# Performance work log

Hardware: AMD Instinct MI355X
Metric: run time of the kernel (lower is better)

The kernel has to match this reference:

```python
import jax, jax.numpy as jnp
import numpy as np
from jax import lax

H = 256  # hidden_size


def _conv1d(x, w, b):
    # x: (N, Cin, L), w: (Cout, Cin, K) -> (N, Cout, L-K+1), VALID, stride 1
    y = lax.conv_general_dilated(x, w, window_strides=(1,), padding='VALID',
                                 dimension_numbers=('NCH', 'OIH', 'NCH'))
    return y + b[None, :, None]


def _gru_dir(x, Wih, Whh, bih, bhh):
    # x: (L, N, H). Torch GRU cell equations.
    L, N, _ = x.shape
    gi = jnp.einsum('lnh,gh->lng', x, Wih) + bih  # (L, N, 3H) precomputed input gates
    h0 = jnp.zeros((N, H), x.dtype)

    def step(h, gi_t):
        gh = h @ Whh.T + bhh                       # (N, 3H)
        ir, iz, inn = jnp.split(gi_t, 3, axis=-1)
        hr, hz, hn = jnp.split(gh, 3, axis=-1)
        r = jax.nn.sigmoid(ir + hr)
        z = jax.nn.sigmoid(iz + hz)
        n = jnp.tanh(inn + r * hn)
        h_new = (1.0 - z) * n + z * h
        return h_new, h_new

    hT, ys = lax.scan(step, h0, gi)
    return ys, hT  # (L, N, H), (N, H)


def setup_inputs() -> dict:
    key = jax.random.key(0)
    ks = jax.random.split(key, 14)
    N, C, L = 32, 13, 4096
    s = 0.1
    inp = {
        'X': jax.random.normal(ks[0], (N, C, L), jnp.float32),
        'W1': jax.random.normal(ks[1], (H // 2, C, 3), jnp.float32) * s,
        'b1': jax.random.normal(ks[2], (H // 2,), jnp.float32) * s,
        'W2': jax.random.normal(ks[3], (H, H // 2, 3), jnp.float32) * s,
        'b2': jax.random.normal(ks[4], (H,), jnp.float32) * s,
        'Wih_f': jax.random.normal(ks[5], (3 * H, H), jnp.float32) * s,
        'Whh_f': jax.random.normal(ks[6], (3 * H, H), jnp.float32) * s,
        'bih_f': jax.random.normal(ks[7], (3 * H,), jnp.float32) * s,
        'bhh_f': jax.random.normal(ks[8], (3 * H,), jnp.float32) * s,
        'Wih_b': jax.random.normal(ks[9], (3 * H, H), jnp.float32) * s,
        'Whh_b': jax.random.normal(ks[10], (3 * H, H), jnp.float32) * s,
        'bih_b': jax.random.normal(ks[11], (3 * H,), jnp.float32) * s,
        'bhh_b': jax.random.normal(ks[12], (3 * H,), jnp.float32) * s,
    }
    return inp


def reference(X, W1, b1, W2, b2, Wih_f, Whh_f, bih_f, bhh_f,
              Wih_b, Whh_b, bih_b, bhh_b):
    # dropouts are identity in eval mode; N>1 so squeeze() is a no-op
    x = _conv1d(X, W1, b1)           # (N, H/2, L-2)
    x = _conv1d(x, W2, b2)           # (N, H,   L-4)
    x = x[:, :, ::2]                 # MaxPool1d(kernel=1, stride=2) == stride-2 subsample
    x = jnp.transpose(x, (2, 0, 1))  # (L', N, H)

    out_f, hT_f = _gru_dir(x, Wih_f, Whh_f, bih_f, bhh_f)
    # backward direction: reverse time, scan, reverse outputs
    out_b_rev, hT_b = _gru_dir(x[::-1], Wih_b, Whh_b, bih_b, bhh_b)
    out_b = out_b_rev[::-1]

    # original: fwd + flip(bwd along FEATURE axis), averaged, ReLU (faithful to np.flip(axis=-1))
    comb = jax.nn.relu((out_f + out_b[:, :, ::-1]) * 0.5)  # (L', N, H)
    hidden_last = hT_b[None]                                # hidden[-1].unsqueeze(0): (1, N, H)
    return comb, hidden_last
```

## Files before the change

kernel.cpp:

```cpp
#include <hip/hip_runtime.h>
#include <hip/hip_fp16.h>
#include <cstdint>
#include <cstddef>

#define L_SEQ 2046
#define NBATCH 32
#define HID 256
#define M_PAD 65536

typedef _Float16 h2vec  __attribute__((ext_vector_type(2)));
typedef _Float16 half8v __attribute__((ext_vector_type(8)));
typedef float    f32x4  __attribute__((ext_vector_type(4)));

static __device__ __forceinline__ uint32_t pack2(float a, float b) {
  __half2 h = __floats2half2_rn(a, b);
  return __builtin_bit_cast(uint32_t, h);
}

static __device__ __forceinline__ float fdot2u(uint32_t w, uint32_t h, float c) {
#if __has_builtin(__builtin_amdgcn_fdot2)
  return __builtin_amdgcn_fdot2(__builtin_bit_cast(h2vec, w),
                                __builtin_bit_cast(h2vec, h), c, false);
#else
  __half2 a = __builtin_bit_cast(__half2, w);
  __half2 b = __builtin_bit_cast(__half2, h);
  float2 fa = __half22float2(a), fb = __half22float2(b);
  return c + fa.x * fb.x + fa.y * fb.y;
#endif
}

static __device__ __forceinline__ void gload_lds16(const void* g, void* l) {
  __builtin_amdgcn_global_load_lds(
      (const __attribute__((address_space(1))) void*)g,
      (__attribute__((address_space(3))) void*)l, 16, 0, 0);
}

__global__ void k_conv_im2col(const float* __restrict__ X,
                              const float* __restrict__ W1,
                              const float* __restrict__ b1,
                              __half* __restrict__ A1h) {
  int j   = threadIdx.x;
  int row = blockIdx.x;
  int l2 = row >> 5, n = row & 31;
  float v = 0.f;
  if (l2 < L_SEQ) {
    int ci = j / 3;
    int k  = j - 3 * ci;
    int p  = 2 * l2 + k;
    const float* xb = X + (size_t)n * 13 * 4096 + p;
    const float* w  = W1 + ci * 39;
    float acc = b1[ci];
#pragma unroll
    for (int c = 0; c < 13; c++) {
      const float* xp = xb + (size_t)c * 4096;
      acc += xp[0] * w[3*c+0] + xp[1] * w[3*c+1] + xp[2] * w[3*c+2];
    }
    v = acc;
  }
  A1h[(size_t)row * 384 + j] = __float2half(v);
}

__global__ void k_cvt_h(const float* __restrict__ src, __half* __restrict__ dst,
                        int nelem) {
  int i = blockIdx.x * 256 + threadIdx.x;
  if (i < nelem) dst[i] = __float2half(src[i]);
}

__global__ __launch_bounds__(256, 3) void k_gemm_mfma(
    const __half* __restrict__ A, const __half* __restrict__ Bh,
    const float* __restrict__ bias, __half* __restrict__ C,
    int K, int ldC, int col_off) {
  __shared__ __half Asl[128 * 64];
  __shared__ __half Bsl[128 * 64];
  const int tid  = threadIdx.x;
  const int wave = tid >> 6, lane = tid & 63;
  const int m_blk = blockIdx.x * 128;
  const int n_blk = blockIdx.y * 128;
  const int wm = wave >> 1, wn = wave & 1;

  f32x4 acc[4][4];
#pragma unroll
  for (int i = 0; i < 4; i++)
#pragma unroll
    for (int j = 0; j < 4; j++) acc[i][j] = (f32x4)0.f;

  int srow[4], sko[4];
#pragma unroll
  for (int i = 0; i < 4; i++) {
    int s = (i * 4 + wave) * 64 + lane;
    srow[i] = s >> 3;
    sko[i]  = (s & 7) ^ ((s >> 3) & 7);
  }

  for (int kc = 0; kc < K; kc += 64) {
#pragma unroll
    for (int i = 0; i < 4; i++) {
      int s = (i * 4 + wave) * 64 + lane;
      gload_lds16(A + (size_t)(m_blk + srow[i]) * K + kc + sko[i] * 8,
                  &Asl[s * 8]);
    }
#pragma unroll
    for (int i = 0; i < 4; i++) {
      int s = (i * 4 + wave) * 64 + lane;
      gload_lds16(Bh + (size_t)(n_blk + srow[i]) * K + kc + sko[i] * 8,
                  &Bsl[s * 8]);
    }
    __syncthreads();
#pragma unroll
    for (int kb = 0; kb < 2; kb++) {
      half8v af[4], bf[4];
#pragma unroll
      for (int mi = 0; mi < 4; mi++) {
        int row = wm * 64 + mi * 16 + (lane & 15);
        int c   = (kb * 4 + (lane >> 4)) ^ (row & 7);
        af[mi] = *(const half8v*)&Asl[row * 64 + c * 8];
      }
#pragma unroll
      for (int ni = 0; ni < 4; ni++) {
        int row = wn * 64 + ni * 16 + (lane & 15);
        int c   = (kb * 4 + (lane >> 4)) ^ (row & 7);
        bf[ni] = *(const half8v*)&Bsl[row * 64 + c * 8];
      }
#pragma unroll
      for (int mi = 0; mi < 4; mi++)
#pragma unroll
        for (int ni = 0; ni < 4; ni++)
          acc[mi][ni] = __builtin_amdgcn_mfma_f32_16x16x32_f16(
              af[mi], bf[ni], acc[mi][ni], 0, 0, 0);
    }
    __syncthreads();
  }
#pragma unroll
  for (int ni = 0; ni < 4; ni++) {
    int col = wn * 64 + ni * 16 + (lane & 15);
    float bj = bias[n_blk + col];
#pragma unroll
    for (int mi = 0; mi < 4; mi++) {
      int row0 = m_blk + wm * 64 + mi * 16 + (lane >> 4) * 4;
#pragma unroll
      for (int r = 0; r < 4; r++) {
        C[(size_t)(row0 + r) * ldC + col_off + n_blk + col] =
            __float2half(acc[mi][ni][r] + bj);
      }
    }
  }
}

__global__ void k_packw2(const float* __restrict__ Whh_f,
                         const float* __restrict__ Whh_b,
                         uint4* __restrict__ Wpk) {
  int idx = blockIdx.x * 256 + threadIdx.x;
  int d   = idx / 24576;
  int r   = idx - d * 24576;
  int w   = r / 768;
  int j   = r - w * 768;
  const float* W = d ? Whh_b : Whh_f;
  const float* src = W + (size_t)j * 256 + w * 8;
  uint4 o;
  o.x = pack2(src[0], src[1]);
  o.y = pack2(src[2], src[3]);
  o.z = pack2(src[4], src[5]);
  o.w = pack2(src[6], src[7]);
  Wpk[(size_t)idx] = o;
}

__global__ __attribute__((amdgpu_flat_work_group_size(768, 768),
                          amdgpu_waves_per_eu(3, 3)))
void k_gru(
    const __half* __restrict__ gih, const uint4* __restrict__ Wpk,
    const float* __restrict__ bhh_f, const float* __restrict__ bhh_b,
    float* __restrict__ outF, __half* __restrict__ outBh,
    float* __restrict__ hT) {
  const int blk = blockIdx.x;
  const int dir = blk >> 5;
  const int n   = blk & 31;
  const int tid = threadIdx.x;
  const int wv_ = tid >> 6;
  const int lane = tid & 63;
  const bool is_act = (wv_ % 3) == 0;
  const int g = (wv_ / 3) * 64 + lane;

  const float* bhh = dir ? bhh_b : bhh_f;

  uint4 wv[32];
  {
    const uint4* wp = Wpk + (size_t)dir * 24576 + tid;
#pragma unroll
    for (int w = 0; w < 32; w++) wv[w] = wp[w * 768];
#pragma unroll
    for (int w = 0; w < 32; w++) {
      asm volatile("" : "+v"(wv[w].x), "+v"(wv[w].y), "+v"(wv[w].z), "+v"(wv[w].w));
    }
  }
  const float bh0 = bhh[g];
  const float bh1 = bhh[256 + g];
  const float bh2 = bhh[512 + g];

  __shared__ __align__(16) __half hs[2][256];
  __shared__ float a_lds[768];
  if (tid < 128) ((uint32_t*)hs)[tid] = 0u;
  float hp = 0.f;

  const __half* gr = gih + ((size_t)(dir ? (size_t)(L_SEQ - 1) * NBATCH : 0) + n) * 1536
                         + dir * 768 + g;
  const ptrdiff_t gstep = dir ? -(ptrdiff_t)(NBATCH * 1536) : (ptrdiff_t)(NBATCH * 1536);
  __half pi0 = __float2half(0.f), pi1 = pi0, pi2 = pi0;
  if (is_act) { pi0 = gr[0]; pi1 = gr[256]; pi2 = gr[512]; }
  __syncthreads();

  for (int t = 0; t < L_SEQ; t++) {
    const uint4* hb = (const uint4*)hs[t & 1];
    float a = 0.f;
#pragma unroll
    for (int w = 0; w < 32; w++) {
      uint4 hq = hb[w];
      uint4 u  = wv[w];
      a = fdot2u(u.x, hq.x, a);
      a = fdot2u(u.y, hq.y, a);
      a = fdot2u(u.z, hq.z, a);
      a = fdot2u(u.w, hq.w, a);
    }
    a_lds[tid] = a;
    __syncthreads();

    if (is_act) {
      float hr = a_lds[g]       + bh0;
      float hz = a_lds[256 + g] + bh1;
      float hn = a_lds[512 + g] + bh2;
      float ir  = __half2float(pi0);
      float iz  = __half2float(pi1);
      float inn = __half2float(pi2);
      float rr = 1.f / (1.f + __expf(-(ir + hr)));
      float zz = 1.f / (1.f + __expf(-(iz + hz)));
      float e  = __expf(2.f * (inn + rr * hn));
      float nn = 1.f - 2.f / (e + 1.f);
      float hnew = (1.f - zz) * nn + zz * hp;
      hp = hnew;
      __half hh = __float2half(hnew);
      hs[(t + 1) & 1][g] = hh;
      const int l = dir ? (L_SEQ - 1 - t) : t;
      uint32_t oi = ((uint32_t)l * NBATCH + n) * HID + g;
      if (dir == 0) outF[oi] = hnew;
      else          outBh[oi] = hh;
      gr += gstep;
      if (t + 1 < L_SEQ) { pi0 = gr[0]; pi1 = gr[256]; pi2 = gr[512]; }
    }
    __syncthreads();
  }
  if (dir == 1 && is_act) hT[n * HID + g] = hp;
}

__global__ void k_combine(float* __restrict__ outF,
                          const __half* __restrict__ outBh) {
  int idx = blockIdx.x * 256 + threadIdx.x;
  int c = idx & 255;
  float v = 0.5f * (outF[idx] + __half2float(outBh[idx + 255 - 2 * c]));
  outF[idx] = v > 0.f ? v : 0.f;
}

extern "C" void kernel_launch(void* const* d_in, const int* in_sizes, int n_in,
                              void* d_out, int out_size, void* d_ws, size_t ws_size,
                              hipStream_t stream) {
  const float* X     = (const float*)d_in[0];
  const float* W1    = (const float*)d_in[1];
  const float* b1    = (const float*)d_in[2];
  const float* W2    = (const float*)d_in[3];
  const float* b2    = (const float*)d_in[4];
  const float* Wih_f = (const float*)d_in[5];
  const float* Whh_f = (const float*)d_in[6];
  const float* bih_f = (const float*)d_in[7];
  const float* bhh_f = (const float*)d_in[8];
  const float* Wih_b = (const float*)d_in[9];
  const float* Whh_b = (const float*)d_in[10];
  const float* bih_b = (const float*)d_in[11];
  const float* bhh_b = (const float*)d_in[12];

  char* wsb = (char*)d_ws;
  __half* gih   = (__half*)(wsb);
  __half* W2h   = (__half*)(wsb);
  __half* A1h   = (__half*)(wsb + 201326592);
  __half* outBh = (__half*)(wsb + 201326592);
  uint4*  Wpk   = (uint4*)(wsb + 234848768);
  __half* WihfH = (__half*)(wsb + 235635200);
  __half* WihbH = (__half*)(wsb + 236028416);

  float*  outF  = (float*)d_out;
  __half* xsubh = (__half*)d_out;
  float*  hT    = outF + (size_t)L_SEQ * NBATCH * HID;

  k_conv_im2col<<<dim3(M_PAD), 384, 0, stream>>>(X, W1, b1, A1h);
  k_cvt_h<<<dim3(384), 256, 0, stream>>>(W2, W2h, 98304);
  k_gemm_mfma<<<dim3(512, 2), 256, 0, stream>>>(A1h, W2h, b2, xsubh, 384, 256, 0);
  k_cvt_h<<<dim3(768), 256, 0, stream>>>(Wih_f, WihfH, 196608);
  k_cvt_h<<<dim3(768), 256, 0, stream>>>(Wih_b, WihbH, 196608);
  k_packw2<<<dim3(192), 256, 0, stream>>>(Whh_f, Whh_b, Wpk);
  k_gemm_mfma<<<dim3(512, 6), 256, 0, stream>>>(xsubh, WihfH, bih_f, gih, 256, 1536, 0);
  k_gemm_mfma<<<dim3(512, 6), 256, 0, stream>>>(xsubh, WihbH, bih_b, gih, 256, 1536, 768);
  k_gru<<<dim3(64), 768, 0, stream>>>(gih, Wpk, bhh_f, bhh_b, outF, outBh, hT);
  k_combine<<<dim3(65472), 256, 0, stream>>>(outF, outBh);
}
```

Before: 3.125 ms.

## Batch 8 sequences per GRU block and compute recurrent matvec with MFMA

The recurrent GRU kernel moves from one block per (direction, batch element) using fdot2 dot products to eight blocks, each handling eight batch elements. The h@Whh step becomes 16x16x32 f16 MFMA tiles, with weights repacked into MFMA fragment layout and kept in registers. The hidden state sits in swizzled LDS, and input-gate rows are prefetched asynchronously into double-buffered LDS. The r/z recurrent biases are folded into the precomputed input-gate bias so the per-step activation does less work. This trades parallelism (only 8 CUs busy) for far fewer instructions per step, and half the MFMA columns are wasted padding.

```diff
diff --git a/kernel.cpp b/kernel.cpp
--- a/kernel.cpp
+++ b/kernel.cpp
@@ -11,22 +11,15 @@
 typedef _Float16 h2vec  __attribute__((ext_vector_type(2)));
 typedef _Float16 half8v __attribute__((ext_vector_type(8)));
 typedef float    f32x4  __attribute__((ext_vector_type(4)));
+typedef unsigned short u16x4 __attribute__((ext_vector_type(4)));
 
 static __device__ __forceinline__ uint32_t pack2(float a, float b) {
   __half2 h = __floats2half2_rn(a, b);
   return __builtin_bit_cast(uint32_t, h);
 }
 
-static __device__ __forceinline__ float fdot2u(uint32_t w, uint32_t h, float c) {
-#if __has_builtin(__builtin_amdgcn_fdot2)
-  return __builtin_amdgcn_fdot2(__builtin_bit_cast(h2vec, w),
-                                __builtin_bit_cast(h2vec, h), c, false);
-#else
-  __half2 a = __builtin_bit_cast(__half2, w);
-  __half2 b = __builtin_bit_cast(__half2, h);
-  float2 fa = __half22float2(a), fb = __half22float2(b);
-  return c + fa.x * fb.x + fa.y * fb.y;
-#endif
+static __device__ __forceinline__ float u16f(unsigned short u) {
+  return __half2float(__builtin_bit_cast(__half, u));
 }
 
 static __device__ __forceinline__ void gload_lds16(const void* g, void* l) {
@@ -66,6 +59,20 @@
   if (i < nelem) dst[i] = __float2half(src[i]);
 }
 
+__global__ void k_biascomb(const float* __restrict__ bih_f,
+                           const float* __restrict__ bhh_f,
+                           const float* __restrict__ bih_b,
+                           const float* __restrict__ bhh_b,
+                           float* __restrict__ outFb, float* __restrict__ outBb) {
+  int i = blockIdx.x * 256 + threadIdx.x;
+  if (i < 768) {
+    float af = i < 512 ? bhh_f[i] : 0.f;
+    float ab = i < 512 ? bhh_b[i] : 0.f;
+    outFb[i] = bih_f[i] + af;
+    outBb[i] = bih_b[i] + ab;
+  }
+}
+
 __global__ __launch_bounds__(256, 3) void k_gemm_mfma(
     const __half* __restrict__ A, const __half* __restrict__ Bh,
     const float* __restrict__ bias, __half* __restrict__ C,
@@ -146,16 +153,22 @@
   }
 }
 
-__global__ void k_packw2(const float* __restrict__ Whh_f,
+__global__ void k_packw3(const float* __restrict__ Whh_f,
                          const float* __restrict__ Whh_b,
                          uint4* __restrict__ Wpk) {
   int idx = blockIdx.x * 256 + threadIdx.x;
   int d   = idx / 24576;
   int r   = idx - d * 24576;
-  int w   = r / 768;
-  int j   = r - w * 768;
+  int w   = r / 3072;
+  int r2  = r - w * 3072;
+  int f   = r2 >> 6;
+  int l   = r2 & 63;
+  int t6  = f >> 3, ks = f & 7;
+  int gate = t6 >> 1, jj = t6 & 1;
+  int row = gate * 256 + w * 32 + jj * 16 + (l & 15);
+  int k0  = ks * 32 + (l >> 4) * 8;
   const float* W = d ? Whh_b : Whh_f;
-  const float* src = W + (size_t)j * 256 + w * 8;
+  const float* src = W + (size_t)row * 256 + k0;
   uint4 o;
   o.x = pack2(src[0], src[1]);
   o.y = pack2(src[2], src[3]);
@@ -164,90 +177,140 @@
   Wpk[(size_t)idx] = o;
 }
 
-__global__ __attribute__((amdgpu_flat_work_group_size(768, 768),
-                          amdgpu_waves_per_eu(3, 3)))
+__global__ __attribute__((amdgpu_flat_work_group_size(512, 512),
+                          amdgpu_waves_per_eu(2, 2)))
 void k_gru(
     const __half* __restrict__ gih, const uint4* __restrict__ Wpk,
     const float* __restrict__ bhh_f, const float* __restrict__ bhh_b,
     float* __restrict__ outF, __half* __restrict__ outBh,
     float* __restrict__ hT) {
   const int blk = blockIdx.x;
-  const int dir = blk >> 5;
-  const int n   = blk & 31;
+  const int dir = blk >> 2;
+  const int n0  = (blk & 3) * 8;
   const int tid = threadIdx.x;
-  const int wv_ = tid >> 6;
-  const int lane = tid & 63;
-  const bool is_act = (wv_ % 3) == 0;
-  const int g = (wv_ / 3) * 64 + lane;
+  const int w   = tid >> 6;
+  const int l   = tid & 63;
+  const int n   = l & 15;
+  const int ng  = n & 7;
+  const int hi  = l >> 4;
+  const bool nvalid = (n < 8);
+
+  uint4 wv[48];
+  {
+    const uint4* wp = Wpk + ((size_t)(dir * 8 + w) * 48) * 64 + l;
+#pragma unroll
+    for (int f = 0; f < 48; f++) wv[f] = wp[f * 64];
+  }
 
   const float* bhh = dir ? bhh_b : bhh_f;
-
-  uint4 wv[32];
+  f32x4 bh2[2];
+  bh2[0] = *(const f32x4*)&bhh[512 + w * 32 + 0 * 16 + hi * 4];
+  bh2[1] = *(const f32x4*)&bhh[512 + w * 32 + 1 * 16 + hi * 4];
+
+  __shared__ __align__(16) __half h_lds[2][16 * 256];
+  __shared__ __align__(16) __half gi_lds[2][8 * 776];
   {
-    const uint4* wp = Wpk + (size_t)dir * 24576 + tid;
-#pragma unroll
-    for (int w = 0; w < 32; w++) wv[w] = wp[w * 768];
-#pragma unroll
-    for (int w = 0; w < 32; w++) {
-      asm volatile("" : "+v"(wv[w].x), "+v"(wv[w].y), "+v"(wv[w].z), "+v"(wv[w].w));
-    }
-  }
-  const float bh0 = bhh[g];
-  const float bh1 = bhh[256 + g];
-  const float bh2 = bhh[512 + g];
-
-  __shared__ __align__(16) __half hs[2][256];
-  __shared__ float a_lds[768];
-  if (tid < 128) ((uint32_t*)hs)[tid] = 0u;
-  float hp = 0.f;
-
-  const __half* gr = gih + ((size_t)(dir ? (size_t)(L_SEQ - 1) * NBATCH : 0) + n) * 1536
-                         + dir * 768 + g;
-  const ptrdiff_t gstep = dir ? -(ptrdiff_t)(NBATCH * 1536) : (ptrdiff_t)(NBATCH * 1536);
-  __half pi0 = __float2half(0.f), pi1 = pi0, pi2 = pi0;
-  if (is_act) { pi0 = gr[0]; pi1 = gr[256]; pi2 = gr[512]; }
+    uint32_t* p = (uint32_t*)h_lds;
+#pragma unroll
+    for (int i = 0; i < 8; i++) p[i * 512 + tid] = 0u;
+  }
+  float hp[2][4];
+#pragma unroll
+  for (int jj = 0; jj < 2; jj++)
+#pragma unroll
+    for (int vv = 0; vv < 4; vv++) hp[jj][vv] = 0.f;
+
+  const size_t gi_rowstep = (size_t)NBATCH * 1536;
+#define STAGE_GI(tt, buf) do {                                              \
+    int lidx_ = dir ? (L_SEQ - 1 - (tt)) : (tt);                            \
+    const char* src_ = (const char*)(gih +                                   \
+        ((size_t)lidx_ * NBATCH + n0 + w) * 1536 + dir * 768);              \
+    char* dst_ = (char*)&gi_lds[buf][w * 776];                              \
+    gload_lds16(src_ + l * 16, dst_ + l * 16);                              \
+    if (l < 32) gload_lds16(src_ + 1024 + l * 16, dst_ + 1024 + l * 16);    \
+  } while (0)
+
+  STAGE_GI(0, 0);
   __syncthreads();
 
+  int cur = 0;
   for (int t = 0; t < L_SEQ; t++) {
-    const uint4* hb = (const uint4*)hs[t & 1];
-    float a = 0.f;
-#pragma unroll
-    for (int w = 0; w < 32; w++) {
-      uint4 hq = hb[w];
-      uint4 u  = wv[w];
-      a = fdot2u(u.x, hq.x, a);
-      a = fdot2u(u.y, hq.y, a);
-      a = fdot2u(u.z, hq.z, a);
-      a = fdot2u(u.w, hq.w, a);
-    }
-    a_lds[tid] = a;
+    if (t + 1 < L_SEQ) STAGE_GI(t + 1, cur ^ 1);
+
+    f32x4 acc[6];
+#pragma unroll
+    for (int i = 0; i < 6; i++) acc[i] = (f32x4)0.f;
+    {
+      const __half* hb = h_lds[cur];
+#pragma unroll
+      for (int ks = 0; ks < 8; ks++) {
+        int c_lin = ks * 4 + hi;
+        int c_swz = (c_lin & 24) | ((c_lin & 7) ^ ng);
+        half8v bf = *(const half8v*)&hb[n * 256 + c_swz * 8];
+#pragma unroll
+        for (int t6 = 0; t6 < 6; t6++)
+          acc[t6] = __builtin_amdgcn_mfma_f32_16x16x32_f16(
+              __builtin_bit_cast(half8v, wv[t6 * 8 + ks]), bf, acc[t6], 0, 0, 0);
+      }
+    }
+
+    const int lidx = dir ? (L_SEQ - 1 - t) : t;
+    const __half* gi = &gi_lds[cur][ng * 776];
+    u16x4 giv[3][2];
+#pragma unroll
+    for (int gt = 0; gt < 3; gt++)
+#pragma unroll
+      for (int jj = 0; jj < 2; jj++)
+        giv[gt][jj] = *(const u16x4*)&gi[gt * 256 + w * 32 + jj * 16 + hi * 4];
+
+#pragma unroll
+    for (int jj = 0; jj < 2; jj++) {
+      float hnew[4];
+#pragma unroll
+      for (int vv = 0; vv < 4; vv++) {
+        float hr = acc[0 + jj][vv];
+        float hz = acc[2 + jj][vv];
+        float hn = acc[4 + jj][vv] + bh2[jj][vv];
+        float ir  = u16f(giv[0][jj][vv]);
+        float iz  = u16f(giv[1][jj][vv]);
+        float inn = u16f(giv[2][jj][vv]);
+        float rr = 1.f / (1.f + __expf(-(ir + hr)));
+        float zz = 1.f / (1.f + __expf(-(iz + hz)));
+        float e  = __expf(2.f * (inn + rr * hn));
+        float nn = 1.f - 2.f / (e + 1.f);
+        hnew[vv] = (1.f - zz) * nn + zz * hp[jj][vv];
+        hp[jj][vv] = hnew[vv];
+      }
+      if (nvalid) {
+        const int gbase = w * 32 + jj * 16 + hi * 4;
+        uint2 pk;
+        pk.x = pack2(hnew[0], hnew[1]);
+        pk.y = pack2(hnew[2], hnew[3]);
+        int c_lin = gbase >> 3;
+        int c_swz = (c_lin & 24) | ((c_lin & 7) ^ ng);
+        *(uint2*)&h_lds[cur ^ 1][n * 256 + c_swz * 8 + (gbase & 7)] = pk;
+        const size_t oi = ((size_t)lidx * NBATCH + n0 + n) * HID + gbase;
+        if (dir == 0) {
+          f32x4 o; o[0] = hnew[0]; o[1] = hnew[1]; o[2] = hnew[2]; o[3] = hnew[3];
+          *(f32x4*)&outF[oi] = o;
+        } else {
+          *(uint2*)&outBh[oi] = pk;
+        }
+      }
+    }
     __syncthreads();
-
-    if (is_act) {
-      float hr = a_lds[g]       + bh0;
-      float hz = a_lds[256 + g] + bh1;
-      float hn = a_lds[512 + g] + bh2;
-      float ir  = __half2float(pi0);
-      float iz  = __half2float(pi1);
-      float inn = __half2float(pi2);
-      float rr = 1.f / (1.f + __expf(-(ir + hr)));
-      float zz = 1.f / (1.f + __expf(-(iz + hz)));
-      float e  = __expf(2.f * (inn + rr * hn));
-      float nn = 1.f - 2.f / (e + 1.f);
-      float hnew = (1.f - zz) * nn + zz * hp;
-      hp = hnew;
-      __half hh = __float2half(hnew);
-      hs[(t + 1) & 1][g] = hh;
-      const int l = dir ? (L_SEQ - 1 - t) : t;
-      uint32_t oi = ((uint32_t)l * NBATCH + n) * HID + g;
-      if (dir == 0) outF[oi] = hnew;
-      else          outBh[oi] = hh;
-      gr += gstep;
-      if (t + 1 < L_SEQ) { pi0 = gr[0]; pi1 = gr[256]; pi2 = gr[512]; }
-    }
-    __syncthreads();
-  }
-  if (dir == 1 && is_act) hT[n * HID + g] = hp;
+    cur ^= 1;
+  }
+
+  if (dir == 1 && nvalid) {
+#pragma unroll
+    for (int jj = 0; jj < 2; jj++) {
+      const int gbase = w * 32 + jj * 16 + hi * 4;
+      f32x4 o; o[0] = hp[jj][0]; o[1] = hp[jj][1]; o[2] = hp[jj][2]; o[3] = hp[jj][3];
+      *(f32x4*)&hT[(size_t)(n0 + n) * HID + gbase] = o;
+    }
+  }
+#undef STAGE_GI
 }
 
 __global__ void k_combine(float* __restrict__ outF,
@@ -280,9 +343,11 @@
   __half* W2h   = (__half*)(wsb);
   __half* A1h   = (__half*)(wsb + 201326592);
   __half* outBh = (__half*)(wsb + 201326592);
-  uint4*  Wpk   = (uint4*)(wsb + 234848768);
+  uint4*  Wpk3  = (uint4*)(wsb + 234848768);
   __half* WihfH = (__half*)(wsb + 235635200);
   __half* WihbH = (__half*)(wsb + 236028416);
+  float*  biasF = (float*)(wsb + 236421632);
+  float*  biasB = (float*)(wsb + 236424704);
 
   float*  outF  = (float*)d_out;
   __half* xsubh = (__half*)d_out;
@@ -293,9 +358,10 @@
   k_gemm_mfma<<<dim3(512, 2), 256, 0, stream>>>(A1h, W2h, b2, xsubh, 384, 256, 0);
   k_cvt_h<<<dim3(768), 256, 0, stream>>>(Wih_f, WihfH, 196608);
   k_cvt_h<<<dim3(768), 256, 0, stream>>>(Wih_b, WihbH, 196608);
-  k_packw2<<<dim3(192), 256, 0, stream>>>(Whh_f, Whh_b, Wpk);
-  k_gemm_mfma<<<dim3(512, 6), 256, 0, stream>>>(xsubh, WihfH, bih_f, gih, 256, 1536, 0);
-  k_gemm_mfma<<<dim3(512, 6), 256, 0, stream>>>(xsubh, WihbH, bih_b, gih, 256, 1536, 768);
-  k_gru<<<dim3(64), 768, 0, stream>>>(gih, Wpk, bhh_f, bhh_b, outF, outBh, hT);
+  k_packw3<<<dim3(192), 256, 0, stream>>>(Whh_f, Whh_b, Wpk3);
+  k_biascomb<<<dim3(3), 256, 0, stream>>>(bih_f, bhh_f, bih_b, bhh_b, biasF, biasB);
+  k_gemm_mfma<<<dim3(512, 6), 256, 0, stream>>>(xsubh, WihfH, biasF, gih, 256, 1536, 0);
+  k_gemm_mfma<<<dim3(512, 6), 256, 0, stream>>>(xsubh, WihbH, biasB, gih, 256, 1536, 768);
+  k_gru<<<dim3(8), 512, 0, stream>>>(gih, Wpk3, bhh_f, bhh_b, outF, outBh, hT);
   k_combine<<<dim3(65472), 256, 0, stream>>>(outF, outBh);
 }
```

After: 7.903 ms. 2.53x slower.
